# Optimization experiments

Measured on AMD Instinct MI355X. Metric: run time of the kernel, lower is better.

## Reference

```python
import jax, jax.numpy as jnp
import numpy as np

SZ = 8192
DEL_NUM = 2048
TEMP = 10.0
EPS = 1e-20
E = DEL_NUM * (2 * SZ - DEL_NUM - 1) // 2  # 14,679,040


def _triu_scatter_indices(sz: int, del_num: int):
    """Row-major (i, j) pairs with i < j and j >= sz - del_num, matching
    torch.triu(left_mask).nonzero() ordering."""
    s = sz - del_num
    # Part 1: rows i in [0, s), cols j in [s, sz)
    rows1 = np.repeat(np.arange(s), del_num)
    cols1 = np.tile(np.arange(s, sz), s)
    # Part 2: strict upper triangle of the bottom-right del_num x del_num block
    ti, tj = np.triu_indices(del_num, k=1)
    rows = np.concatenate([rows1, ti + s]).astype(np.int32)
    cols = np.concatenate([cols1, tj + s]).astype(np.int32)
    return jnp.asarray(rows), jnp.asarray(cols)


def setup_inputs() -> dict:
    key = jax.random.key(0)
    k1, k2 = jax.random.split(key)
    gen_matrix = jax.random.normal(k1, (E, 2), dtype=jnp.float32)
    u = jax.random.uniform(k2, (E, 2), dtype=jnp.float32)
    return {"gen_matrix": gen_matrix, "u": u, "sz": SZ, "del_num": DEL_NUM}


def reference(gen_matrix, u, sz, del_num):
    # Gumbel noise from uniform samples (matches gumbel_sample)
    gumbel = -jnp.log(-jnp.log(u + EPS) + EPS)
    # gumbel_softmax_sample, soft path (hard=False)
    y = jax.nn.softmax((gen_matrix + gumbel) / TEMP, axis=1)
    out = y[:, 0]  # [E]
    rows, cols = _triu_scatter_indices(sz, del_num)
    matrix = jnp.zeros((sz, sz), dtype=out.dtype).at[rows, cols].set(out)
    return matrix + matrix.T
```

## Files before the change

kernel.cpp:

```cpp
#include <hip/hip_runtime.h>
#include <cstddef>

#define SZ    8192
#define DELN  2048
#define SOFF  6144
#define BASE2 12582912
#define TINV  0.1f
#define FEPS  1e-20f

__device__ __forceinline__ float gsig(float a0, float a1, float u0, float u1) {
    float g0 = -__logf(-__logf(u0 + FEPS) + FEPS);
    float g1 = -__logf(-__logf(u1 + FEPS) + FEPS);
    float d  = (a0 + g0 - a1 - g1) * TINV;
    return __fdividef(1.0f, 1.0f + __expf(-d));
}

__global__ __launch_bounds__(256) void k_zero(float* __restrict__ out) {
    int c4  = blockIdx.x * 256 + threadIdx.x;
    int row = blockIdx.y;
    *(float4*)(out + (size_t)row * SZ + (size_t)c4 * 4) = make_float4(0.f, 0.f, 0.f, 0.f);
}

__global__ __launch_bounds__(256) void k_tr(const float* __restrict__ gen,
                                            const float* __restrict__ uu,
                                            float* __restrict__ out) {
    __shared__ float tile[64][65];
    const int tJ = blockIdx.x;
    const int tI = blockIdx.y;
    const int i0 = tI * 64;
    const int jb = tJ * 64;
    const int c4 = threadIdx.x & 15;
    const int r  = threadIdx.x >> 4;
    const int lc = c4 * 4;

    #pragma unroll
    for (int it = 0; it < 4; ++it) {
        const int li = r + 16 * it;
        const int i  = i0 + li;
        const size_t e0 = (size_t)i * DELN + (size_t)(jb + lc);
        const float4* gp = (const float4*)(gen + 2 * e0);
        const float4* up = (const float4*)(uu  + 2 * e0);
        float4 ga = gp[0], gb = gp[1];
        float4 ua = up[0], ub = up[1];
        float v0 = gsig(ga.x, ga.y, ua.x, ua.y);
        float v1 = gsig(ga.z, ga.w, ua.z, ua.w);
        float v2 = gsig(gb.x, gb.y, ub.x, ub.y);
        float v3 = gsig(gb.z, gb.w, ub.z, ub.w);
        tile[li][lc] = v0; tile[li][lc+1] = v1; tile[li][lc+2] = v2; tile[li][lc+3] = v3;
        *(float4*)(out + (size_t)i * SZ + (size_t)(SOFF + jb + lc)) =
            make_float4(v0, v1, v2, v3);
    }
    __syncthreads();
    #pragma unroll
    for (int it = 0; it < 4; ++it) {
        const int lj  = r + 16 * it;
        const int row = SOFF + jb + lj;
        float4 v = make_float4(tile[lc][lj], tile[lc+1][lj], tile[lc+2][lj], tile[lc+3][lj]);
        *(float4*)(out + (size_t)row * SZ + (size_t)(i0 + lc)) = v;
    }
}

__device__ __forceinline__ long br_base(int ti) {
    return (long)BASE2 + (long)ti * (DELN - 1) - ((long)ti * (ti - 1)) / 2 - (long)ti - 1;
}

__global__ __launch_bounds__(256) void k_br(const float* __restrict__ gen,
                                            const float* __restrict__ uu,
                                            float* __restrict__ out) {
    __shared__ float tile[64][65];
    int rem = blockIdx.x;
    int tI = 0;
    while (rem >= 32 - tI) { rem -= 32 - tI; ++tI; }
    const int tJ  = tI + rem;
    const int ti0 = tI * 64;
    const int tj0 = tJ * 64;
    const int c4  = threadIdx.x & 15;
    const int r   = threadIdx.x >> 4;
    const int lc  = c4 * 4;
    const bool diag = (tI == tJ);

    #pragma unroll
    for (int it = 0; it < 4; ++it) {
        const int li = r + 16 * it;
        const int ti = ti0 + li;
        const long eb = br_base(ti) + (long)(tj0 + lc);
        float v[4];
        #pragma unroll
        for (int k = 0; k < 4; ++k) {
            const int tj = tj0 + lc + k;
            if (!diag || ti < tj) {
                const long e = eb + k;
                float2 g = *(const float2*)(gen + 2 * e);
                float2 w = *(const float2*)(uu  + 2 * e);
                v[k] = gsig(g.x, g.y, w.x, w.y);
            } else {
                v[k] = 0.0f;
            }
        }
        tile[li][lc] = v[0]; tile[li][lc+1] = v[1]; tile[li][lc+2] = v[2]; tile[li][lc+3] = v[3];
        if (!diag) {
            *(float4*)(out + (size_t)(SOFF + ti) * SZ + (size_t)(SOFF + tj0 + lc)) =
                make_float4(v[0], v[1], v[2], v[3]);
        }
    }
    __syncthreads();
    if (diag) {
        #pragma unroll
        for (int it = 0; it < 4; ++it) {
            const int li = r + 16 * it;
            float4 v;
            float* pv = &v.x;
            #pragma unroll
            for (int k = 0; k < 4; ++k) {
                const int ltj = lc + k;
                pv[k] = (li <= ltj) ? tile[li][ltj] : tile[ltj][li];
            }
            *(float4*)(out + (size_t)(SOFF + ti0 + li) * SZ + (size_t)(SOFF + tj0 + lc)) = v;
        }
    } else {
        #pragma unroll
        for (int it = 0; it < 4; ++it) {
            const int lj = r + 16 * it;
            float4 v = make_float4(tile[lc][lj], tile[lc+1][lj], tile[lc+2][lj], tile[lc+3][lj]);
            *(float4*)(out + (size_t)(SOFF + tj0 + lj) * SZ + (size_t)(SOFF + ti0 + lc)) = v;
        }
    }
}

extern "C" void kernel_launch(void* const* d_in, const int* in_sizes, int n_in,
                              void* d_out, int out_size, void* d_ws, size_t ws_size,
                              hipStream_t stream) {
    const float* gen = (const float*)d_in[0];
    const float* uu  = (const float*)d_in[1];
    float* out = (float*)d_out;

    k_zero<<<dim3(6, 6144), 256, 0, stream>>>(out);
    k_tr<<<dim3(32, 96), 256, 0, stream>>>(gen, uu, out);
    k_br<<<dim3(528), 256, 0, stream>>>(gen, uu, out);
}
```

Before: 428.7 us.

## Fuse zero-fill, rectangle, and triangle kernels into one interleaved launch

```diff
diff --git a/kernel.cpp b/kernel.cpp
--- a/kernel.cpp
+++ b/kernel.cpp
@@ -8,6 +8,11 @@
 #define TINV  0.1f
 #define FEPS  1e-20f
 
+#define NBR   528
+#define NTR   3072
+#define NZ    1536
+#define NGRID (NBR + NTR + NZ)
+
 __device__ __forceinline__ float gsig(float a0, float a1, float u0, float u1) {
     float g0 = -__logf(-__logf(u0 + FEPS) + FEPS);
     float g1 = -__logf(-__logf(u1 + FEPS) + FEPS);
@@ -15,68 +20,75 @@
     return __fdividef(1.0f, 1.0f + __expf(-d));
 }
 
-__global__ __launch_bounds__(256) void k_zero(float* __restrict__ out) {
-    int c4  = blockIdx.x * 256 + threadIdx.x;
-    int row = blockIdx.y;
-    *(float4*)(out + (size_t)row * SZ + (size_t)c4 * 4) = make_float4(0.f, 0.f, 0.f, 0.f);
-}
-
-__global__ __launch_bounds__(256) void k_tr(const float* __restrict__ gen,
-                                            const float* __restrict__ uu,
-                                            float* __restrict__ out) {
-    __shared__ float tile[64][65];
-    const int tJ = blockIdx.x;
-    const int tI = blockIdx.y;
-    const int i0 = tI * 64;
-    const int jb = tJ * 64;
-    const int c4 = threadIdx.x & 15;
-    const int r  = threadIdx.x >> 4;
-    const int lc = c4 * 4;
-
-    #pragma unroll
-    for (int it = 0; it < 4; ++it) {
-        const int li = r + 16 * it;
-        const int i  = i0 + li;
-        const size_t e0 = (size_t)i * DELN + (size_t)(jb + lc);
-        const float4* gp = (const float4*)(gen + 2 * e0);
-        const float4* up = (const float4*)(uu  + 2 * e0);
-        float4 ga = gp[0], gb = gp[1];
-        float4 ua = up[0], ub = up[1];
-        float v0 = gsig(ga.x, ga.y, ua.x, ua.y);
-        float v1 = gsig(ga.z, ga.w, ua.z, ua.w);
-        float v2 = gsig(gb.x, gb.y, ub.x, ub.y);
-        float v3 = gsig(gb.z, gb.w, ub.z, ub.w);
-        tile[li][lc] = v0; tile[li][lc+1] = v1; tile[li][lc+2] = v2; tile[li][lc+3] = v3;
-        *(float4*)(out + (size_t)i * SZ + (size_t)(SOFF + jb + lc)) =
-            make_float4(v0, v1, v2, v3);
-    }
-    __syncthreads();
-    #pragma unroll
-    for (int it = 0; it < 4; ++it) {
-        const int lj  = r + 16 * it;
-        const int row = SOFF + jb + lj;
-        float4 v = make_float4(tile[lc][lj], tile[lc+1][lj], tile[lc+2][lj], tile[lc+3][lj]);
-        *(float4*)(out + (size_t)row * SZ + (size_t)(i0 + lc)) = v;
-    }
-}
-
 __device__ __forceinline__ long br_base(int ti) {
     return (long)BASE2 + (long)ti * (DELN - 1) - ((long)ti * (ti - 1)) / 2 - (long)ti - 1;
 }
 
-__global__ __launch_bounds__(256) void k_br(const float* __restrict__ gen,
-                                            const float* __restrict__ uu,
-                                            float* __restrict__ out) {
+__global__ __launch_bounds__(256) void k_fused(const float* __restrict__ gen,
+                                               const float* __restrict__ uu,
+                                               float* __restrict__ out) {
     __shared__ float tile[64][65];
-    int rem = blockIdx.x;
+    const int bid = blockIdx.x;
+    const int c4  = threadIdx.x & 15;
+    const int r   = threadIdx.x >> 4;
+    const int lc  = c4 * 4;
+
+    if (bid >= NBR) {
+        const int b2 = bid - NBR;
+        const int g  = b2 / 3;
+        const int p  = b2 - g * 3;
+
+        if (p == 2) {
+            const int lane = threadIdx.x & 63;
+            const int w    = threadIdx.x >> 6;
+            float4* rowp = (float4*)(out + (size_t)(g * 4 + w) * SZ);
+            const float4 z4 = make_float4(0.f, 0.f, 0.f, 0.f);
+            #pragma unroll
+            for (int k = 0; k < 24; ++k)
+                rowp[k * 64 + lane] = z4;
+            return;
+        }
+
+        const int t  = g * 2 + p;
+        const int tJ = t & 31;
+        const int tI = t >> 5;
+        const int i0 = tI * 64;
+        const int jb = tJ * 64;
+
+        #pragma unroll
+        for (int it = 0; it < 4; ++it) {
+            const int li = r + 16 * it;
+            const int i  = i0 + li;
+            const size_t e0 = (size_t)i * DELN + (size_t)(jb + lc);
+            const float4* gp = (const float4*)(gen + 2 * e0);
+            const float4* up = (const float4*)(uu  + 2 * e0);
+            float4 ga = gp[0], gb = gp[1];
+            float4 ua = up[0], ub = up[1];
+            float v0 = gsig(ga.x, ga.y, ua.x, ua.y);
+            float v1 = gsig(ga.z, ga.w, ua.z, ua.w);
+            float v2 = gsig(gb.x, gb.y, ub.x, ub.y);
+            float v3 = gsig(gb.z, gb.w, ub.z, ub.w);
+            tile[li][lc] = v0; tile[li][lc+1] = v1; tile[li][lc+2] = v2; tile[li][lc+3] = v3;
+            *(float4*)(out + (size_t)i * SZ + (size_t)(SOFF + jb + lc)) =
+                make_float4(v0, v1, v2, v3);
+        }
+        __syncthreads();
+        #pragma unroll
+        for (int it = 0; it < 4; ++it) {
+            const int lj  = r + 16 * it;
+            const int row = SOFF + jb + lj;
+            float4 v = make_float4(tile[lc][lj], tile[lc+1][lj], tile[lc+2][lj], tile[lc+3][lj]);
+            *(float4*)(out + (size_t)row * SZ + (size_t)(i0 + lc)) = v;
+        }
+        return;
+    }
+
+    int rem = bid;
     int tI = 0;
     while (rem >= 32 - tI) { rem -= 32 - tI; ++tI; }
     const int tJ  = tI + rem;
     const int ti0 = tI * 64;
     const int tj0 = tJ * 64;
-    const int c4  = threadIdx.x & 15;
-    const int r   = threadIdx.x >> 4;
-    const int lc  = c4 * 4;
     const bool diag = (tI == tJ);
 
     #pragma unroll
@@ -134,7 +146,5 @@
     const float* uu  = (const float*)d_in[1];
     float* out = (float*)d_out;
 
-    k_zero<<<dim3(6, 6144), 256, 0, stream>>>(out);
-    k_tr<<<dim3(32, 96), 256, 0, stream>>>(gen, uu, out);
-    k_br<<<dim3(528), 256, 0, stream>>>(gen, uu, out);
+    k_fused<<<dim3(NGRID), 256, 0, stream>>>(gen, uu, out);
 }
```

After: 416.2 us. 1.03x faster.
